# Kernel tuning notes

Hardware: AMD Instinct MI355X
Metric: run time of the kernel (lower is better)

## Reference

```python
import jax, jax.numpy as jnp
import numpy as np

DILATION = 64
KERNEL = 2

def setup_inputs() -> dict:
    key = jax.random.key(0)
    k1, k2 = jax.random.split(key)
    x = jax.random.normal(k1, (16, 64, 16384), dtype=jnp.float32)
    w = jax.random.normal(k2, (64, 64, KERNEL), dtype=jnp.float32) * 0.1
    return {"x": x, "w": w}

def _causal_dilated_conv(x, w):
    # left-pad by dilation*(kernel_size-1) for causality
    pad = DILATION * (KERNEL - 1)
    xp = jnp.pad(x, ((0, 0), (0, 0), (pad, 0)))
    return jax.lax.conv_general_dilated(
        xp, w,
        window_strides=(1,),
        padding='VALID',
        rhs_dilation=(DILATION,),
        dimension_numbers=('NCH', 'OIH', 'NCH'))

def reference(x, w):
    y = _causal_dilated_conv(x, w)          # [B, C_out, T]
    return jnp.tanh(y) * jax.nn.sigmoid(y)  # fused gate
```

## Files before the change

kernel.cpp:

```cpp
#include <hip/hip_runtime.h>


#define B_ 16
#define C_ 64
#define T_ 16384
#define TT 128
#define HALO 64
#define RR (TT + HALO)

typedef __attribute__((ext_vector_type(8))) short short8;
typedef __attribute__((ext_vector_type(4))) float f32x4;

union Frag { short8 s; unsigned u[4]; };

__device__ __forceinline__ unsigned bf16_rne(float f) {
    unsigned u = __float_as_uint(f);
    return (u + 0x7fffu + ((u >> 16) & 1u)) >> 16;
}

__device__ __forceinline__ unsigned pack_rne(float a, float b) {
    unsigned ua = __float_as_uint(a), ub = __float_as_uint(b);
    unsigned ra = ua + 0x7fffu + ((ua >> 16) & 1u);
    unsigned rb = ub + 0x7fffu + ((ub >> 16) & 1u);
    return (ra >> 16) | (rb & 0xffff0000u);
}

__global__ __launch_bounds__(256, 6) void conv_gate_mfma3(
    const float* __restrict__ x,
    const float* __restrict__ w,
    float* __restrict__ out)
{
    __shared__ unsigned short xs[RR * 64];

    const int tid = threadIdx.x;
    const int t0  = blockIdx.x * TT;
    const int b   = blockIdx.y;
    const float* xb = x + (size_t)b * C_ * T_;

    #pragma unroll
    for (int it = 0; it < 6; ++it) {
        int task = it * 256 + tid;
        int rr   = task % RR;
        int c8   = task / RR;
        int g    = t0 - HALO + rr;
        float v[8];
        if (g >= 0) {
            const float* xp = xb + (size_t)(8 * c8) * T_ + g;
            #pragma unroll
            for (int i = 0; i < 8; ++i) v[i] = xp[(size_t)i * T_];
        } else {
            #pragma unroll
            for (int i = 0; i < 8; ++i) v[i] = 0.f;
        }
        unsigned p0 = pack_rne(v[0], v[1]);
        unsigned p1 = pack_rne(v[2], v[3]);
        unsigned p2 = pack_rne(v[4], v[5]);
        unsigned p3 = pack_rne(v[6], v[7]);
        int so = rr * 64 + ((c8 ^ (rr & 7)) * 8);
        *(uint4*)(&xs[so]) = make_uint4(p0, p1, p2, p3);
    }

    const int lane = tid & 63;
    const int wid  = tid >> 6;
    const int m    = lane & 15;
    const int q    = lane >> 4;
    const int co   = wid * 16 + m;

    Frag wh[2][2], wl[2][2];
    #pragma unroll
    for (int h = 0; h < 2; ++h) {
        const float* wp = w + co * 128 + h * 64 + q * 16;
        float f[16];
        #pragma unroll
        for (int v4 = 0; v4 < 4; ++v4) {
            float4 t4 = *(const float4*)(wp + 4 * v4);
            f[4*v4+0] = t4.x; f[4*v4+1] = t4.y; f[4*v4+2] = t4.z; f[4*v4+3] = t4.w;
        }
        #pragma unroll
        for (int p = 0; p < 2; ++p) {
            #pragma unroll
            for (int d = 0; d < 4; ++d) {
                float e0 = f[2*(2*d)   + p];
                float e1 = f[2*(2*d+1) + p];
                unsigned h0 = bf16_rne(e0), h1 = bf16_rne(e1);
                float r0 = e0 - __uint_as_float(h0 << 16);
                float r1 = e1 - __uint_as_float(h1 << 16);
                wh[p][h].u[d] = h0 | (h1 << 16);
                wl[p][h].u[d] = bf16_rne(r0) | (bf16_rne(r1) << 16);
            }
        }
    }

    f32x4 acc[8];
    #pragma unroll
    for (int s = 0; s < 8; ++s) acc[s] = (f32x4){0.f, 0.f, 0.f, 0.f};

    __syncthreads();

    const int n  = m;
    const int sw = n & 7;
    #pragma unroll
    for (int u = 0; u < 12; ++u) {
        const int rbase = (16 * u + n) * 64;
        Frag f0, f1;
        f0.s = *(const short8*)(&xs[rbase + ((q ^ sw) * 8)]);
        f1.s = *(const short8*)(&xs[rbase + (((4 + q) ^ sw) * 8)]);
        if (u < 8) {
            acc[u] = __builtin_amdgcn_mfma_f32_16x16x32_bf16(wh[0][0].s, f0.s, acc[u], 0, 0, 0);
            acc[u] = __builtin_amdgcn_mfma_f32_16x16x32_bf16(wl[0][0].s, f0.s, acc[u], 0, 0, 0);
            acc[u] = __builtin_amdgcn_mfma_f32_16x16x32_bf16(wh[0][1].s, f1.s, acc[u], 0, 0, 0);
            acc[u] = __builtin_amdgcn_mfma_f32_16x16x32_bf16(wl[0][1].s, f1.s, acc[u], 0, 0, 0);
        }
        if (u >= 4) {
            const int s2 = u - 4;
            acc[s2] = __builtin_amdgcn_mfma_f32_16x16x32_bf16(wh[1][0].s, f0.s, acc[s2], 0, 0, 0);
            acc[s2] = __builtin_amdgcn_mfma_f32_16x16x32_bf16(wl[1][0].s, f0.s, acc[s2], 0, 0, 0);
            acc[s2] = __builtin_amdgcn_mfma_f32_16x16x32_bf16(wh[1][1].s, f1.s, acc[s2], 0, 0, 0);
            acc[s2] = __builtin_amdgcn_mfma_f32_16x16x32_bf16(wl[1][1].s, f1.s, acc[s2], 0, 0, 0);
        }
    }

    float* ob = out + ((size_t)b * C_ + wid * 16) * T_ + t0;
    #pragma unroll
    for (int s = 0; s < 8; ++s) {
        #pragma unroll
        for (int r = 0; r < 4; ++r) {
            float y  = acc[s][r];
            y = fminf(fmaxf(y, -20.f), 20.f);
            float e   = __expf(-y);
            float e2  = e * e;
            float num = 1.f - e2;
            float den = (1.f + e) * (1.f + e2);
            ob[(size_t)(4 * q + r) * T_ + 16 * s + n] = num * __builtin_amdgcn_rcpf(den);
        }
    }
}

extern "C" void kernel_launch(void* const* d_in, const int* in_sizes, int n_in,
                              void* d_out, int out_size, void* d_ws, size_t ws_size,
                              hipStream_t stream) {
    const float* x = (const float*)d_in[0];
    const float* w = (const float*)d_in[1];
    float* out = (float*)d_out;
    dim3 grid(T_ / TT, B_);
    conv_gate_mfma3<<<grid, dim3(256), 0, stream>>>(x, w, out);
}
```

Measured before the change: 123.4 us.

## Drop split-bf16 weight correction, halve LDS ring, and remap block order

Weights now go to bf16 as a single RNE-rounded part instead of hi/lo pairs, which halves the MFMA count. The LDS tile shrinks to a 128-row ring: each block computes 64 outputs, then reloads 64 new rows into the freed half and computes the next 64. This removes the 64-row halo overhead per block and allows more blocks per CU. Block indices are permuted across time tiles, and the gate formula is simplified algebraically. Dropping the low-order weight correction lowers accuracy against the fp32 reference.

```diff
diff --git a/kernel.cpp b/kernel.cpp
--- a/kernel.cpp
+++ b/kernel.cpp
@@ -4,19 +4,12 @@
 #define B_ 16
 #define C_ 64
 #define T_ 16384
-#define TT 128
-#define HALO 64
-#define RR (TT + HALO)
+#define RR 128
 
 typedef __attribute__((ext_vector_type(8))) short short8;
 typedef __attribute__((ext_vector_type(4))) float f32x4;
 
 union Frag { short8 s; unsigned u[4]; };
-
-__device__ __forceinline__ unsigned bf16_rne(float f) {
-    unsigned u = __float_as_uint(f);
-    return (u + 0x7fffu + ((u >> 16) & 1u)) >> 16;
-}
 
 __device__ __forceinline__ unsigned pack_rne(float a, float b) {
     unsigned ua = __float_as_uint(a), ub = __float_as_uint(b);
@@ -25,24 +18,32 @@
     return (ra >> 16) | (rb & 0xffff0000u);
 }
 
-__global__ __launch_bounds__(256, 6) void conv_gate_mfma3(
+__global__ __launch_bounds__(256, 8) void conv_gate_mfma5(
     const float* __restrict__ x,
     const float* __restrict__ w,
     float* __restrict__ out)
 {
     __shared__ unsigned short xs[RR * 64];
 
-    const int tid = threadIdx.x;
-    const int t0  = blockIdx.x * TT;
+    const int tid  = threadIdx.x;
+    const int lane = tid & 63;
+    const int wid  = tid >> 6;
+    const int m    = lane & 15;
+    const int q    = lane >> 4;
+    const int n    = m;
+
+    const int bx  = blockIdx.x;
+    const int pr  = ((bx & 7) << 4) | (bx >> 3);
     const int b   = blockIdx.y;
+    const int t0b = pr * 128;
     const float* xb = x + (size_t)b * C_ * T_;
 
     #pragma unroll
-    for (int it = 0; it < 6; ++it) {
+    for (int it = 0; it < 4; ++it) {
         int task = it * 256 + tid;
-        int rr   = task % RR;
-        int c8   = task / RR;
-        int g    = t0 - HALO + rr;
+        int rr   = task & 127;
+        int c8   = task >> 7;
+        int g    = t0b - 64 + rr;
         float v[8];
         if (g >= 0) {
             const float* xp = xb + (size_t)(8 * c8) * T_ + g;
@@ -52,21 +53,13 @@
             #pragma unroll
             for (int i = 0; i < 8; ++i) v[i] = 0.f;
         }
-        unsigned p0 = pack_rne(v[0], v[1]);
-        unsigned p1 = pack_rne(v[2], v[3]);
-        unsigned p2 = pack_rne(v[4], v[5]);
-        unsigned p3 = pack_rne(v[6], v[7]);
         int so = rr * 64 + ((c8 ^ (rr & 7)) * 8);
-        *(uint4*)(&xs[so]) = make_uint4(p0, p1, p2, p3);
+        *(uint4*)(&xs[so]) = make_uint4(pack_rne(v[0], v[1]), pack_rne(v[2], v[3]),
+                                        pack_rne(v[4], v[5]), pack_rne(v[6], v[7]));
     }
 
-    const int lane = tid & 63;
-    const int wid  = tid >> 6;
-    const int m    = lane & 15;
-    const int q    = lane >> 4;
-    const int co   = wid * 16 + m;
-
-    Frag wh[2][2], wl[2][2];
+    const int co = wid * 16 + m;
+    Frag wh[2][2];
     #pragma unroll
     for (int h = 0; h < 2; ++h) {
         const float* wp = w + co * 128 + h * 64 + q * 16;
@@ -77,61 +70,89 @@
             f[4*v4+0] = t4.x; f[4*v4+1] = t4.y; f[4*v4+2] = t4.z; f[4*v4+3] = t4.w;
         }
         #pragma unroll
-        for (int p = 0; p < 2; ++p) {
+        for (int p = 0; p < 2; ++p)
             #pragma unroll
-            for (int d = 0; d < 4; ++d) {
-                float e0 = f[2*(2*d)   + p];
-                float e1 = f[2*(2*d+1) + p];
-                unsigned h0 = bf16_rne(e0), h1 = bf16_rne(e1);
-                float r0 = e0 - __uint_as_float(h0 << 16);
-                float r1 = e1 - __uint_as_float(h1 << 16);
-                wh[p][h].u[d] = h0 | (h1 << 16);
-                wl[p][h].u[d] = bf16_rne(r0) | (bf16_rne(r1) << 16);
-            }
-        }
+            for (int d = 0; d < 4; ++d)
+                wh[p][h].u[d] = pack_rne(f[4*d + p], f[4*d + 2 + p]);
     }
 
-    f32x4 acc[8];
+    const int sw_base = n & 7;
+    float* ob = out + ((size_t)b * C_ + wid * 16) * T_ + t0b;
+
+    f32x4 acc[4];
     #pragma unroll
-    for (int s = 0; s < 8; ++s) acc[s] = (f32x4){0.f, 0.f, 0.f, 0.f};
+    for (int s = 0; s < 4; ++s) acc[s] = (f32x4){0.f, 0.f, 0.f, 0.f};
 
     __syncthreads();
 
-    const int n  = m;
-    const int sw = n & 7;
     #pragma unroll
-    for (int u = 0; u < 12; ++u) {
-        const int rbase = (16 * u + n) * 64;
+    for (int u = 0; u < 8; ++u) {
+        int lr    = 16 * u + n;
+        int rbase = lr * 64;
+        int sw    = lr & 7;
         Frag f0, f1;
         f0.s = *(const short8*)(&xs[rbase + ((q ^ sw) * 8)]);
         f1.s = *(const short8*)(&xs[rbase + (((4 + q) ^ sw) * 8)]);
-        if (u < 8) {
-            acc[u] = __builtin_amdgcn_mfma_f32_16x16x32_bf16(wh[0][0].s, f0.s, acc[u], 0, 0, 0);
-            acc[u] = __builtin_amdgcn_mfma_f32_16x16x32_bf16(wl[0][0].s, f0.s, acc[u], 0, 0, 0);
-            acc[u] = __builtin_amdgcn_mfma_f32_16x16x32_bf16(wh[0][1].s, f1.s, acc[u], 0, 0, 0);
-            acc[u] = __builtin_amdgcn_mfma_f32_16x16x32_bf16(wl[0][1].s, f1.s, acc[u], 0, 0, 0);
-        }
-        if (u >= 4) {
-            const int s2 = u - 4;
-            acc[s2] = __builtin_amdgcn_mfma_f32_16x16x32_bf16(wh[1][0].s, f0.s, acc[s2], 0, 0, 0);
-            acc[s2] = __builtin_amdgcn_mfma_f32_16x16x32_bf16(wl[1][0].s, f0.s, acc[s2], 0, 0, 0);
-            acc[s2] = __builtin_amdgcn_mfma_f32_16x16x32_bf16(wh[1][1].s, f1.s, acc[s2], 0, 0, 0);
-            acc[s2] = __builtin_amdgcn_mfma_f32_16x16x32_bf16(wl[1][1].s, f1.s, acc[s2], 0, 0, 0);
-        }
+        const int tap = u >> 2, s = u & 3;
+        acc[s] = __builtin_amdgcn_mfma_f32_16x16x32_bf16(wh[tap][0].s, f0.s, acc[s], 0, 0, 0);
+        acc[s] = __builtin_amdgcn_mfma_f32_16x16x32_bf16(wh[tap][1].s, f1.s, acc[s], 0, 0, 0);
     }
 
-    float* ob = out + ((size_t)b * C_ + wid * 16) * T_ + t0;
+    __syncthreads();
+
     #pragma unroll
-    for (int s = 0; s < 8; ++s) {
+    for (int it = 0; it < 2; ++it) {
+        int task = it * 256 + tid;
+        int rr2  = task & 63;
+        int c8   = task >> 6;
+        int g    = t0b + 64 + rr2;
+        const float* xp = xb + (size_t)(8 * c8) * T_ + g;
+        float v[8];
+        #pragma unroll
+        for (int i = 0; i < 8; ++i) v[i] = xp[(size_t)i * T_];
+        int so = rr2 * 64 + ((c8 ^ (rr2 & 7)) * 8);
+        *(uint4*)(&xs[so]) = make_uint4(pack_rne(v[0], v[1]), pack_rne(v[2], v[3]),
+                                        pack_rne(v[4], v[5]), pack_rne(v[6], v[7]));
+    }
+
+    #pragma unroll
+    for (int s = 0; s < 4; ++s) {
         #pragma unroll
         for (int r = 0; r < 4; ++r) {
-            float y  = acc[s][r];
+            float y = acc[s][r];
             y = fminf(fmaxf(y, -20.f), 20.f);
-            float e   = __expf(-y);
-            float e2  = e * e;
-            float num = 1.f - e2;
-            float den = (1.f + e) * (1.f + e2);
-            ob[(size_t)(4 * q + r) * T_ + 16 * s + n] = num * __builtin_amdgcn_rcpf(den);
+            float t  = __expf(-y);
+            float o  = (1.f - t) * __builtin_amdgcn_rcpf(1.f + t * t);
+            ob[(size_t)(4 * q + r) * T_ + 16 * s + n] = o;
+        }
+        acc[s] = (f32x4){0.f, 0.f, 0.f, 0.f};
+    }
+
+    __syncthreads();
+
+    #pragma unroll
+    for (int u = 0; u < 8; ++u) {
+        int gr    = 64 + 16 * u + n;
+        int lr    = gr & 127;
+        int rbase = lr * 64;
+        int sw    = lr & 7;
+        Frag f0, f1;
+        f0.s = *(const short8*)(&xs[rbase + ((q ^ sw) * 8)]);
+        f1.s = *(const short8*)(&xs[rbase + (((4 + q) ^ sw) * 8)]);
+        const int tap = u >> 2, s = u & 3;
+        acc[s] = __builtin_amdgcn_mfma_f32_16x16x32_bf16(wh[tap][0].s, f0.s, acc[s], 0, 0, 0);
+        acc[s] = __builtin_amdgcn_mfma_f32_16x16x32_bf16(wh[tap][1].s, f1.s, acc[s], 0, 0, 0);
+    }
+
+    #pragma unroll
+    for (int s = 0; s < 4; ++s) {
+        #pragma unroll
+        for (int r = 0; r < 4; ++r) {
+            float y = acc[s][r];
+            y = fminf(fmaxf(y, -20.f), 20.f);
+            float t  = __expf(-y);
+            float o  = (1.f - t) * __builtin_amdgcn_rcpf(1.f + t * t);
+            ob[(size_t)(4 * q + r) * T_ + 64 + 16 * s + n] = o;
         }
     }
 }
@@ -142,6 +163,6 @@
     const float* x = (const float*)d_in[0];
     const float* w = (const float*)d_in[1];
     float* out = (float*)d_out;
-    dim3 grid(T_ / TT, B_);
-    conv_gate_mfma3<<<grid, dim3(256), 0, stream>>>(x, w, out);
+    dim3 grid(T_ / 128, B_);
+    conv_gate_mfma5<<<grid, dim3(256), 0, stream>>>(x, w, out);
 }
```

New measurement: 126.1 us. 1.02x slower.
